# Optimization experiments

Measured on AMD Instinct MI355X. Metric: run time of the kernel, lower is better.

Reference implementation:

```python
import jax, jax.numpy as jnp
import numpy as np

N = 256
IL_MMI = 0.02      # insertion loss MMI
IMB = 0.01         # imbalance MMI
IL_CR = 0.02       # insertion loss Crossing
CT = 0.01          # cross talk Crossing


def _mmi_matrix():
    # 2x2 MMI: sqrt(1-IL)*[[t, i r],[i r, t]] with t=sqrt((1+imb)/2), r=sqrt((1-imb)/2)
    a = np.sqrt(1.0 - IL_MMI)
    t = np.sqrt((1.0 + IMB) / 2.0)
    r = np.sqrt((1.0 - IMB) / 2.0)
    mmi2 = a * np.array([[t, 1j * r], [1j * r, t]], dtype=np.complex64)
    # block-diagonal over even pairs (0,1),(2,3),...
    return jnp.asarray(np.kron(np.eye(N // 2, dtype=np.complex64), mmi2))


def _crossing_matrix():
    # pairs start at odd index 1; rows 0 and N-1 pass through with amplitude sqrt(1-IL)*sqrt(1-CT)
    a = np.sqrt(1.0 - IL_CR)
    thru = a * np.sqrt(1.0 - CT)
    cr2 = a * np.array([[np.sqrt(CT), 1j * np.sqrt(1.0 - CT)],
                        [1j * np.sqrt(1.0 - CT), np.sqrt(CT)]], dtype=np.complex64)
    M = np.zeros((N, N), dtype=np.complex64)
    M[0, 0] = thru
    for i in range(1, N - 1, 2):
        M[i:i + 2, i:i + 2] = cr2
    if N % 2 == 0:
        M[-1, -1] = thru
    return jnp.asarray(M)


def setup_inputs() -> dict:
    key = jax.random.key(0)
    thetas = jax.random.uniform(key, (N // 2 + 2, N), dtype=jnp.float32) * (2.0 * np.pi)
    return {"thetas": thetas}


def reference(thetas):
    MMI = _mmi_matrix()
    CR = _crossing_matrix()
    phases = jnp.exp(1j * thetas)  # [N//2+2, N] complex64; diag phase-shift layers

    # arch = ht[0] @ I  (diagonal left-multiply == row scaling)
    arch0 = jnp.diag(phases[0])

    def body(arch, ph):
        # one mesh stage with trailing crossing (iterations i = 0 .. N//2-2)
        arch = MMI @ arch
        arch = ph[:, None] * arch      # ht[i+1] @ arch
        arch = MMI @ arch
        arch = CR @ arch
        return arch, None

    arch, _ = jax.lax.scan(body, arch0, phases[1:N // 2])

    # last loop iteration (i = N//2-1): no crossing
    arch = MMI @ arch
    arch = phases[N // 2][:, None] * arch
    arch = MMI @ arch
    # final phase layer ht[N//2+1]
    arch = phases[N // 2 + 1][:, None] * arch
    return arch
```

## Files before the change

kernel.cpp:

```cpp
#include <hip/hip_runtime.h>


__device__ __forceinline__ float dpp_up1(float x) {
    return __int_as_float(__builtin_amdgcn_update_dpp(
        __float_as_int(x), __float_as_int(x), 0x138, 0xf, 0xf, false));
}
__device__ __forceinline__ float dpp_dn1(float x) {
    return __int_as_float(__builtin_amdgcn_update_dpp(
        __float_as_int(x), __float_as_int(x), 0x130, 0xf, 0xf, false));
}

__device__ __forceinline__ void sincos4(float4 th, float sn[4], float cs[4]) {
    __sincosf(th.x, &sn[0], &cs[0]);
    __sincosf(th.y, &sn[1], &cs[1]);
    __sincosf(th.z, &sn[2], &cs[2]);
    __sincosf(th.w, &sn[3], &cs[3]);
}

struct Coef {
    float Er[2], Ei[2], Fr[2], Fi[2], Gr[2], Gi[2];
};

__global__ __launch_bounds__(64)
void neuropuls_mesh_kernel(const float* __restrict__ thetas,
                           float* __restrict__ out)
{
    constexpr int N = 256;
    const int lane = threadIdx.x;
    const int col  = blockIdx.x;

    const float U  = 0.98f * 0.505f;
    const float W  = 0.98f * 0.495f;
    const float Gc = 0.98f * sqrtf(0.505f * 0.495f);
    const float BT = sqrtf(0.98f * 0.01f);
    const float BR = sqrtf(0.98f * 0.99f);

    float vr[4] = {0.f, 0.f, 0.f, 0.f};
    float vi[4] = {0.f, 0.f, 0.f, 0.f};

    {
        const float th0 = thetas[col];
        float s0, c0;
        __sincosf(th0, &s0, &c0);
        const int r0 = col - 4 * lane;
        if (0 <= r0 && r0 < 4) { vr[r0] = c0; vi[r0] = s0; }
    }

    const float* tp = thetas + N + 4 * lane;

    auto prep4 = [&](float4 th, Coef& K) {
        float s[4], c[4];
        sincos4(th, s, c);
        #pragma unroll
        for (int p = 0; p < 2; ++p) {
            const float c0 = c[2 * p], c1 = c[2 * p + 1];
            const float s0 = s[2 * p], s1 = s[2 * p + 1];
            K.Er[p] = U * c0 - W * c1;   K.Ei[p] = U * s0 - W * s1;
            K.Fr[p] = U * c1 - W * c0;   K.Fi[p] = U * s1 - W * s0;
            K.Gr[p] = -Gc * (s0 + s1);   K.Gi[p] = Gc * (c0 + c1);
        }
    };

    auto mstep = [&](const Coef& K) {
        #pragma unroll
        for (int p = 0; p < 2; ++p) {
            const int x = 2 * p, y = 2 * p + 1;
            const float xr = vr[x], xi = vi[x], yr = vr[y], yi = vi[y];
            vr[x] = K.Er[p] * xr - K.Ei[p] * xi + K.Gr[p] * yr - K.Gi[p] * yi;
            vi[x] = K.Er[p] * xi + K.Ei[p] * xr + K.Gr[p] * yi + K.Gi[p] * yr;
            vr[y] = K.Gr[p] * xr - K.Gi[p] * xi + K.Fr[p] * yr - K.Fi[p] * yi;
            vi[y] = K.Gr[p] * xi + K.Gi[p] * xr + K.Fr[p] * yi + K.Fi[p] * yr;
        }
    };

    auto crossing = [&]() {
        float pv3r = dpp_up1(vr[3]);
        float pv3i = dpp_up1(vi[3]);
        float nv0r = dpp_dn1(vr[0]);
        float nv0i = dpp_dn1(vi[0]);
        {
            float xr = vr[1], xi = vi[1], yr = vr[2], yi = vi[2];
            vr[1] = BT * xr - BR * yi;  vi[1] = BT * xi + BR * yr;
            vr[2] = BT * yr - BR * xi;  vi[2] = BT * yi + BR * xr;
        }
        {
            float yr = vr[0], yi = vi[0];
            float nr = BT * yr - BR * pv3i;
            float ni = BT * yi + BR * pv3r;
            vr[0] = (lane == 0) ? BR * yr : nr;
            vi[0] = (lane == 0) ? BR * yi : ni;
        }
        {
            float xr = vr[3], xi = vi[3];
            float nr = BT * xr - BR * nv0i;
            float ni = BT * xi + BR * nv0r;
            vr[3] = (lane == 63) ? BR * xr : nr;
            vi[3] = (lane == 63) ? BR * xi : ni;
        }
    };

    Coef KA;
    float4 thB, thC;
    {
        float4 t1 = *(const float4*)tp;  tp += N;
        thB       = *(const float4*)tp;  tp += N;
        thC       = *(const float4*)tp;  tp += N;
        prep4(t1, KA);
    }

    #pragma unroll 2
    for (int s = 1; s <= 126; ++s) {
        float4 thD = *(const float4*)tp;  tp += N;
        Coef KB;
        prep4(thB, KB);
        mstep(KA);
        crossing();
        KA = KB;
        thB = thC; thC = thD;
    }

    mstep(KA);
    crossing();

    {
        Coef KF;
        prep4(thB, KF);
        mstep(KF);
        float sn[4], cs[4];
        sincos4(thC, sn, cs);
        #pragma unroll
        for (int j = 0; j < 4; ++j) {
            float r = vr[j], i = vi[j];
            vr[j] = cs[j] * r - sn[j] * i;
            vi[j] = cs[j] * i + sn[j] * r;
        }
    }

    #pragma unroll
    for (int j = 0; j < 4; ++j) {
        const int idx = (4 * lane + j) * N + col;
        out[idx]         = vr[j];
        out[N * N + idx] = vi[j];
    }
}

extern "C" void kernel_launch(void* const* d_in, const int* in_sizes, int n_in,
                              void* d_out, int out_size, void* d_ws, size_t ws_size,
                              hipStream_t stream)
{
    const float* thetas = (const float*)d_in[0];
    float* out = (float*)d_out;
    (void)in_sizes; (void)n_in; (void)out_size; (void)d_ws; (void)ws_size;
    neuropuls_mesh_kernel<<<dim3(256), dim3(64), 0, stream>>>(thetas, out);
}
```

Measured before the change: 82.94 us.

## Split mesh into 8 parallel stage groups and combine via complex GEMM tree

The 128-stage serial sweep is replaced by 8 independent groups of 16 stages, each computed by 2048 blocks as a partial transfer matrix written to workspace. Three tree-reduction complex matrix multiply launches then combine the partial matrices, and the final phase layer is applied in the last GEMM. This removes the long serial dependency chain that left only 256 wavefronts active. In exchange it adds roughly 7 dense 256x256 complex GEMMs, extra global memory traffic and three additional kernel launches.

```diff
diff --git a/kernel.cpp b/kernel.cpp
--- a/kernel.cpp
+++ b/kernel.cpp
@@ -9,7 +9,6 @@
     return __int_as_float(__builtin_amdgcn_update_dpp(
         __float_as_int(x), __float_as_int(x), 0x130, 0xf, 0xf, false));
 }
-
 __device__ __forceinline__ void sincos4(float4 th, float sn[4], float cs[4]) {
     __sincosf(th.x, &sn[0], &cs[0]);
     __sincosf(th.y, &sn[1], &cs[1]);
@@ -17,17 +16,16 @@
     __sincosf(th.w, &sn[3], &cs[3]);
 }
 
-struct Coef {
-    float Er[2], Ei[2], Fr[2], Fi[2], Gr[2], Gi[2];
-};
+struct Coef { float Er[2], Ei[2], Fr[2], Fi[2], Gr[2], Gi[2]; };
 
 __global__ __launch_bounds__(64)
-void neuropuls_mesh_kernel(const float* __restrict__ thetas,
-                           float* __restrict__ out)
+void group_kernel(const float* __restrict__ thetas,
+                  float* __restrict__ ws)
 {
-    constexpr int N = 256;
+    const int gid  = blockIdx.x;
+    const int g    = gid >> 8;
+    const int col  = gid & 255;
     const int lane = threadIdx.x;
-    const int col  = blockIdx.x;
 
     const float U  = 0.98f * 0.505f;
     const float W  = 0.98f * 0.495f;
@@ -39,40 +37,41 @@
     float vi[4] = {0.f, 0.f, 0.f, 0.f};
 
     {
-        const float th0 = thetas[col];
-        float s0, c0;
-        __sincosf(th0, &s0, &c0);
         const int r0 = col - 4 * lane;
-        if (0 <= r0 && r0 < 4) { vr[r0] = c0; vi[r0] = s0; }
-    }
-
-    const float* tp = thetas + N + 4 * lane;
+        if (0 <= r0 && r0 < 4) {
+            if (g == 0) {
+                float s0, c0;
+                __sincosf(thetas[col], &s0, &c0);
+                vr[r0] = c0; vi[r0] = s0;
+            } else {
+                vr[r0] = 1.f;
+            }
+        }
+    }
 
     auto prep4 = [&](float4 th, Coef& K) {
         float s[4], c[4];
         sincos4(th, s, c);
         #pragma unroll
         for (int p = 0; p < 2; ++p) {
-            const float c0 = c[2 * p], c1 = c[2 * p + 1];
-            const float s0 = s[2 * p], s1 = s[2 * p + 1];
+            const float c0 = c[2*p], c1 = c[2*p+1];
+            const float s0 = s[2*p], s1 = s[2*p+1];
             K.Er[p] = U * c0 - W * c1;   K.Ei[p] = U * s0 - W * s1;
             K.Fr[p] = U * c1 - W * c0;   K.Fi[p] = U * s1 - W * s0;
             K.Gr[p] = -Gc * (s0 + s1);   K.Gi[p] = Gc * (c0 + c1);
         }
     };
-
     auto mstep = [&](const Coef& K) {
         #pragma unroll
         for (int p = 0; p < 2; ++p) {
-            const int x = 2 * p, y = 2 * p + 1;
+            const int x = 2*p, y = 2*p+1;
             const float xr = vr[x], xi = vi[x], yr = vr[y], yi = vi[y];
-            vr[x] = K.Er[p] * xr - K.Ei[p] * xi + K.Gr[p] * yr - K.Gi[p] * yi;
-            vi[x] = K.Er[p] * xi + K.Ei[p] * xr + K.Gr[p] * yi + K.Gi[p] * yr;
-            vr[y] = K.Gr[p] * xr - K.Gi[p] * xi + K.Fr[p] * yr - K.Fi[p] * yi;
-            vi[y] = K.Gr[p] * xi + K.Gi[p] * xr + K.Fr[p] * yi + K.Fi[p] * yr;
+            vr[x] = K.Er[p]*xr - K.Ei[p]*xi + K.Gr[p]*yr - K.Gi[p]*yi;
+            vi[x] = K.Er[p]*xi + K.Ei[p]*xr + K.Gr[p]*yi + K.Gi[p]*yr;
+            vr[y] = K.Gr[p]*xr - K.Gi[p]*xi + K.Fr[p]*yr - K.Fi[p]*yi;
+            vi[y] = K.Gr[p]*xi + K.Gi[p]*xr + K.Fr[p]*yi + K.Fi[p]*yr;
         }
     };
-
     auto crossing = [&]() {
         float pv3r = dpp_up1(vr[3]);
         float pv3i = dpp_up1(vi[3]);
@@ -80,67 +79,112 @@
         float nv0i = dpp_dn1(vi[0]);
         {
             float xr = vr[1], xi = vi[1], yr = vr[2], yi = vi[2];
-            vr[1] = BT * xr - BR * yi;  vi[1] = BT * xi + BR * yr;
-            vr[2] = BT * yr - BR * xi;  vi[2] = BT * yi + BR * xr;
+            vr[1] = BT*xr - BR*yi;  vi[1] = BT*xi + BR*yr;
+            vr[2] = BT*yr - BR*xi;  vi[2] = BT*yi + BR*xr;
         }
         {
             float yr = vr[0], yi = vi[0];
-            float nr = BT * yr - BR * pv3i;
-            float ni = BT * yi + BR * pv3r;
-            vr[0] = (lane == 0) ? BR * yr : nr;
-            vi[0] = (lane == 0) ? BR * yi : ni;
+            float nr = BT*yr - BR*pv3i;
+            float ni = BT*yi + BR*pv3r;
+            vr[0] = (lane == 0) ? BR*yr : nr;
+            vi[0] = (lane == 0) ? BR*yi : ni;
         }
         {
             float xr = vr[3], xi = vi[3];
-            float nr = BT * xr - BR * nv0i;
-            float ni = BT * xi + BR * nv0r;
-            vr[3] = (lane == 63) ? BR * xr : nr;
-            vi[3] = (lane == 63) ? BR * xi : ni;
+            float nr = BT*xr - BR*nv0i;
+            float ni = BT*xi + BR*nv0r;
+            vr[3] = (lane == 63) ? BR*xr : nr;
+            vi[3] = (lane == 63) ? BR*xi : ni;
         }
     };
 
-    Coef KA;
-    float4 thB, thC;
-    {
-        float4 t1 = *(const float4*)tp;  tp += N;
-        thB       = *(const float4*)tp;  tp += N;
-        thC       = *(const float4*)tp;  tp += N;
-        prep4(t1, KA);
-    }
-
-    #pragma unroll 2
-    for (int s = 1; s <= 126; ++s) {
-        float4 thD = *(const float4*)tp;  tp += N;
-        Coef KB;
-        prep4(thB, KB);
-        mstep(KA);
-        crossing();
-        KA = KB;
-        thB = thC; thC = thD;
-    }
-
-    mstep(KA);
-    crossing();
-
-    {
-        Coef KF;
-        prep4(thB, KF);
-        mstep(KF);
-        float sn[4], cs[4];
-        sincos4(thC, sn, cs);
-        #pragma unroll
-        for (int j = 0; j < 4; ++j) {
-            float r = vr[j], i = vi[j];
-            vr[j] = cs[j] * r - sn[j] * i;
-            vi[j] = cs[j] * i + sn[j] * r;
-        }
-    }
-
-    #pragma unroll
-    for (int j = 0; j < 4; ++j) {
-        const int idx = (4 * lane + j) * N + col;
-        out[idx]         = vr[j];
-        out[N * N + idx] = vi[j];
+    const float* tp = thetas + (16*g + 1) * 256 + 4 * lane;
+    float4 th = *(const float4*)tp;
+    for (int k = 0; k < 16; ++k) {
+        float4 thn = *(const float4*)(tp + (k + 1) * 256);
+        Coef K;
+        prep4(th, K);
+        mstep(K);
+        if (16*g + 1 + k != 128) crossing();
+        th = thn;
+    }
+
+    float* base = ws + g * 131072;
+    float4 re = make_float4(vr[0], vr[1], vr[2], vr[3]);
+    float4 im = make_float4(vi[0], vi[1], vi[2], vi[3]);
+    *(float4*)(base + col * 256 + 4 * lane)         = re;
+    *(float4*)(base + 65536 + col * 256 + 4 * lane) = im;
+}
+
+__global__ __launch_bounds__(256)
+void cgemm_kernel(float* __restrict__ ws,
+                  const float* __restrict__ thetas,
+                  float* __restrict__ out,
+                  int level)
+{
+    __shared__ float As_re[16][68], As_im[16][68];
+    __shared__ float Bs_re[16][68], Bs_im[16][68];
+
+    const int t  = threadIdx.x;
+    const int bx = blockIdx.x;
+    const int b  = blockIdx.y;
+    const int br = bx & 15, bc = bx >> 4;
+    const int tr = t & 15,  tc = t >> 4;
+
+    const float* A; const float* B; float* C = nullptr;
+    if (level == 0) {
+        A = ws + (2*b + 1) * 131072;
+        B = ws + (2*b) * 131072;
+        C = ws + 1048576 + b * 131072;
+    } else if (level == 1) {
+        A = ws + 1048576 + (2*b + 1) * 131072;
+        B = ws + 1048576 + (2*b) * 131072;
+        C = ws + 1572864 + b * 131072;
+    } else {
+        A = ws + 1572864 + 131072;
+        B = ws + 1572864;
+    }
+
+    const int r = br * 16 + tr;
+    const int c = bc * 16 + tc;
+    float accr = 0.f, acci = 0.f;
+
+    for (int k0 = 0; k0 < 256; k0 += 64) {
+        #pragma unroll
+        for (int i = 0; i < 4; ++i) {
+            const int e  = t + i * 256;
+            const int rr = e & 15, kk = e >> 4;
+            const int ga = (k0 + kk) * 256 + br * 16 + rr;
+            As_re[rr][kk] = A[ga];
+            As_im[rr][kk] = A[65536 + ga];
+        }
+        #pragma unroll
+        for (int i = 0; i < 4; ++i) {
+            const int e  = t + i * 256;
+            const int kk = e & 63, cc = e >> 6;
+            const int gb = (bc * 16 + cc) * 256 + k0 + kk;
+            Bs_re[cc][kk] = B[gb];
+            Bs_im[cc][kk] = B[65536 + gb];
+        }
+        __syncthreads();
+        #pragma unroll 4
+        for (int kk = 0; kk < 64; ++kk) {
+            const float ar = As_re[tr][kk], ai = As_im[tr][kk];
+            const float xr = Bs_re[tc][kk], xi = Bs_im[tc][kk];
+            accr += ar * xr - ai * xi;
+            acci += ar * xi + ai * xr;
+        }
+        __syncthreads();
+    }
+
+    if (level < 2) {
+        C[c * 256 + r]         = accr;
+        C[65536 + c * 256 + r] = acci;
+    } else {
+        float s9, c9;
+        __sincosf(thetas[129 * 256 + r], &s9, &c9);
+        out[r * 256 + c]         = c9 * accr - s9 * acci;
+        out[65536 + r * 256 + c] = c9 * acci + s9 * accr;
     }
 }
 
@@ -150,6 +194,11 @@
 {
     const float* thetas = (const float*)d_in[0];
     float* out = (float*)d_out;
-    (void)in_sizes; (void)n_in; (void)out_size; (void)d_ws; (void)ws_size;
-    neuropuls_mesh_kernel<<<dim3(256), dim3(64), 0, stream>>>(thetas, out);
-}
+    float* ws  = (float*)d_ws;
+    (void)in_sizes; (void)n_in; (void)out_size; (void)ws_size;
+
+    group_kernel<<<dim3(2048), dim3(64), 0, stream>>>(thetas, ws);
+    cgemm_kernel<<<dim3(256, 4), dim3(256), 0, stream>>>(ws, thetas, out, 0);
+    cgemm_kernel<<<dim3(256, 2), dim3(256), 0, stream>>>(ws, thetas, out, 1);
+    cgemm_kernel<<<dim3(256, 1), dim3(256), 0, stream>>>(ws, thetas, out, 2);
+}
```

After: 126.1 us. +52.0%, slower.
